# Kernel tuning notes

Measured on AMD Instinct MI355X. Metric: run time of the kernel, lower is better.

## Reference

```python
import jax, jax.numpy as jnp
import numpy as np

B, BAG, H, C = 512, 32, 1024, 53
EPS = 1e-8  # torch F.cosine_similarity denominator clamp


def setup_inputs() -> dict:
    key = jax.random.key(0)
    ks = jax.random.split(key, 5)
    return {
        "sent_reps": jax.random.normal(ks[0], (B, BAG, H), jnp.float32),
        "aug_sent_reps": jax.random.normal(ks[1], (B, BAG, H), jnp.float32),
        "rel_table": jax.random.normal(ks[2], (C, H), jnp.float32),
        "cls_w": jax.random.normal(ks[3], (C, H), jnp.float32) * 0.02,
        "cls_b": jnp.zeros((C,), jnp.float32),
        "labels": jax.random.randint(ks[4], (B,), 0, C),
        "temperature": jnp.asarray(0.1, jnp.float32),
    }


def _cl(rep, aug, bag_rep, T):
    # rep, aug: (B, bag, H); bag_rep: (B, H)
    nr = jnp.linalg.norm(rep, axis=-1)        # (B, bag)
    na = jnp.linalg.norm(aug, axis=-1)        # (B, bag)
    nb = jnp.linalg.norm(bag_rep, axis=-1)    # (B,)
    pos_sim = jnp.sum(rep * aug, axis=-1) / jnp.maximum(nr * na, EPS)  # (B, bag)
    pos = jnp.exp(pos_sim / T)
    # pair[c, j, b] = cos(rep[b, j], bag_rep[c])  -- matches torch permute/broadcast chain
    dots = jnp.einsum('bjh,ch->cjb', rep, bag_rep)               # (B, bag, B)
    denom = jnp.maximum(nb[:, None, None] * nr.T[None], EPS)      # (B, bag, B)
    pair = dots / denom
    idx = jnp.arange(rep.shape[0])
    axis_sim = pair[idx, :, idx]                                  # (B, bag): cos(rep[b,j], bag_rep[b])
    neg = jnp.exp(pair / T).sum(axis=2) - jnp.exp(axis_sim / T)   # (B, bag)
    return jnp.mean(-jnp.log(pos / (pos + neg)))


def reference(sent_reps, aug_sent_reps, rel_table, cls_w, cls_b, labels, temperature):
    # Selective attention per bag (scope slices are uniform bags of size BAG -> vectorized)
    rel = rel_table[labels]                                        # (B, H)
    scale = jnp.sqrt(jnp.asarray(H, sent_reps.dtype))
    scores = jnp.einsum('bh,bjh->bj', rel, sent_reps) / scale      # (B, bag)
    alphas = jax.nn.softmax(scores, axis=-1)
    bag_reps = jnp.einsum('bj,bjh->bh', alphas, sent_reps)         # (B, H)
    bag_out = bag_reps @ cls_w.T + cls_b                           # (B, C)  (dropout in eval = identity)
    cl_loss = _cl(sent_reps, aug_sent_reps, bag_reps, temperature)
    return bag_out, cl_loss
```

## Files before the change

### kernel.cpp

```cpp
#include <hip/hip_runtime.h>
#include <hip/hip_bf16.h>


typedef __bf16 bf16x8 __attribute__((ext_vector_type(8)));
typedef __bf16 bf16x4 __attribute__((ext_vector_type(4)));
typedef __bf16 bf16x2 __attribute__((ext_vector_type(2)));
typedef float  f32x4  __attribute__((ext_vector_type(4)));

__device__ inline float wsum(float v) {
    #pragma unroll
    for (int off = 32; off > 0; off >>= 1) v += __shfl_xor(v, off, 64);
    return v;
}

__device__ inline void gll16(const void* g, void* l) {
    __builtin_amdgcn_global_load_lds((const __attribute__((address_space(1))) void*)g,
                                     (__attribute__((address_space(3))) void*)l, 16, 0, 0);
}

__device__ inline f32x4 ntld(const float* p) {
    return __builtin_nontemporal_load((const f32x4*)p);
}

__global__ __launch_bounds__(512, 4) void kab(
    const float* __restrict__ sent, const float* __restrict__ aug,
    const float* __restrict__ rel_table, const int* __restrict__ labels,
    __bf16* __restrict__ repb, float* __restrict__ nr, float* __restrict__ pos_sim,
    const float* __restrict__ clsw, __bf16* __restrict__ cwb,
    __bf16* __restrict__ bagb, float* __restrict__ nbsq, float* __restrict__ loss)
{
    __shared__ __align__(16) __bf16 repS[32][1024];
    __shared__ float scoreS[32], alphaS[32], redS[8];
    const int b = blockIdx.x, t = threadIdx.x;
    const int w = t >> 6, lane = t & 63;

    if (b < 128) {
        const int i = b * 512 + t;
        cwb[i] = (i < 53 * 1024) ? (__bf16)clsw[i] : (__bf16)0.0f;
        if (b == 0 && t == 0) *loss = 0.0f;
    }

    const float* relp = rel_table + (size_t)labels[b] * 1024;
    #pragma unroll
    for (int rr = 0; rr < 4; rr++) {
        const int j = w * 4 + rr;
        const size_t rbase = ((size_t)b * 32 + j) * 1024;
        const float* srow = sent + rbase;
        const float* arow = aug + rbase;
        float P = 0.f, R = 0.f, A = 0.f, D = 0.f;
        #pragma unroll
        for (int i = 0; i < 4; i++) {
            const int h = i * 256 + lane * 4;
            f32x4 v  = ntld(srow + h);
            f32x4 a  = ntld(arow + h);
            f32x4 rl = *(const f32x4*)(relp + h);
            P += v.x * rl.x + v.y * rl.y + v.z * rl.z + v.w * rl.w;
            R += v.x * v.x + v.y * v.y + v.z * v.z + v.w * v.w;
            A += a.x * a.x + a.y * a.y + a.z * a.z + a.w * a.w;
            D += v.x * a.x + v.y * a.y + v.z * a.z + v.w * a.w;
            bf16x4 vb = { (__bf16)v.x, (__bf16)v.y, (__bf16)v.z, (__bf16)v.w };
            *(bf16x4*)(&repS[j][h]) = vb;
            *(bf16x4*)(repb + rbase + h) = vb;
        }
        #pragma unroll
        for (int off = 32; off > 0; off >>= 1) {
            P += __shfl_xor(P, off, 64);
            R += __shfl_xor(R, off, 64);
            A += __shfl_xor(A, off, 64);
            D += __shfl_xor(D, off, 64);
        }
        if (lane == 0) {
            scoreS[j] = P * (1.0f / 32.0f);
            float nrv = sqrtf(R), nav = sqrtf(A);
            nr[b * 32 + j] = nrv;
            pos_sim[b * 32 + j] = D / fmaxf(nrv * nav, 1e-8f);
        }
    }
    __syncthreads();

    if (t < 32) {
        float sj = scoreS[t], mx = sj;
        #pragma unroll
        for (int off = 16; off > 0; off >>= 1) mx = fmaxf(mx, __shfl_xor(mx, off, 32));
        float e = __expf(sj - mx), sm = e;
        #pragma unroll
        for (int off = 16; off > 0; off >>= 1) sm += __shfl_xor(sm, off, 32);
        alphaS[t] = e / sm;
    }
    __syncthreads();

    float b0 = 0.f, b1 = 0.f;
    #pragma unroll 8
    for (int j = 0; j < 32; j++) {
        const float al = alphaS[j];
        bf16x2 v = *(const bf16x2*)(&repS[j][t * 2]);
        b0 += al * (float)v.x;
        b1 += al * (float)v.y;
    }
    bf16x2 bb = { (__bf16)b0, (__bf16)b1 };
    *(bf16x2*)(bagb + (size_t)b * 1024 + t * 2) = bb;

    float q = b0 * b0 + b1 * b1;
    q = wsum(q);
    if (lane == 0) redS[w] = q;
    __syncthreads();
    if (t == 0)
        nbsq[b] = redS[0] + redS[1] + redS[2] + redS[3]
                + redS[4] + redS[5] + redS[6] + redS[7];
}

__global__ __launch_bounds__(512, 4) void k4_gemm(
    const __bf16* __restrict__ repb, const __bf16* __restrict__ bagb,
    const float* __restrict__ nr, const float* __restrict__ nbsq,
    const float* __restrict__ temp, float* __restrict__ partial, float* __restrict__ diag,
    const __bf16* __restrict__ cwb, const float* __restrict__ bias, float* __restrict__ out)
{
    __shared__ __align__(16) char smem[65536];
    const int bid = blockIdx.x;
    const int t = threadIdx.x, lane = t & 63, w = t >> 6;
    const int m = lane & 15, quad = lane >> 4;

    if (bid >= 512) {
        __bf16* Al = (__bf16*)smem;
        __bf16* Bl = (__bf16*)(smem + 8192);
        const int r0 = (bid - 512) * 64;
        f32x4 acc[4] = {};
        const int i0 = (t & 255) * 8;
        const int row0 = i0 >> 5, kk0 = i0 & 31;
        const __bf16* gA = bagb + (size_t)(r0 + row0) * 1024 + kk0;
        const __bf16* gB = cwb + (size_t)row0 * 1024 + kk0;
        const bool act = (t < 256);
        for (int k0 = 0; k0 < 1024; k0 += 64) {
            __syncthreads();
            if (act) {
                gll16(gA + k0,      Al + i0);
                gll16(gA + k0 + 32, Al + 2048 + i0);
                gll16(gB + k0,      Bl + i0);
                gll16(gB + k0 + 32, Bl + 2048 + i0);
            }
            __syncthreads();
            if (act) {
                #pragma unroll
                for (int ks = 0; ks < 2; ks++) {
                    bf16x8 a = *(const bf16x8*)(&Al[ks * 2048 + (w * 16 + m) * 32 + quad * 8]);
                    #pragma unroll
                    for (int n = 0; n < 4; n++) {
                        bf16x8 bf = *(const bf16x8*)(&Bl[ks * 2048 + (n * 16 + m) * 32 + quad * 8]);
                        acc[n] = __builtin_amdgcn_mfma_f32_16x16x32_bf16(a, bf, acc[n], 0, 0, 0);
                    }
                }
            }
        }
        if (act) {
            #pragma unroll
            for (int n = 0; n < 4; n++) {
                const int c = n * 16 + m;
                if (c < 53) {
                    #pragma unroll
                    for (int i = 0; i < 4; i++) {
                        const int r = r0 + w * 16 + quad * 4 + i;
                        out[(size_t)r * 53 + c] = acc[n][i] + bias[c];
                    }
                }
            }
        }
        return;
    }

    float (*negp)[32][128] = (float (*)[32][128])(smem + 32768);

    const int xcd = bid & 7, slot = bid >> 3;
    const int cb = slot & 3, rb = (slot >> 2) * 8 + xcd;
    const int r0 = rb * 128, c0 = cb * 128;
    const int wr0 = (w & 1) * 64, wc0 = (w >> 1) * 32;
    const int half = w & 1;

    const int tt = t & 255;
    const bool isB = (t >= 256);
    const int srow = tt >> 2;
    const int scol = 8 * ((tt & 3) ^ ((srow >> 1) & 3));
    const __bf16* g0 = (isB ? bagb + (size_t)(c0 + srow) * 1024
                            : repb + (size_t)(r0 + srow) * 1024) + scol;
    const __bf16* g1 = g0 + 64 * 1024;
    const int d0 = (isB ? 4096 : 0) + tt * 8;
    const int d1 = d0 + 2048;

    const int rho = (m >> 1) & 3;
    const int offA = ((wr0 + m) * 4 + (quad ^ rho)) * 8;
    const int offB = 4096 + ((wc0 + m) * 4 + (quad ^ rho)) * 8;

    f32x4 acc[4][2] = {};

    #define BUFB(s) ((__bf16*)(smem + (((s) & 3) << 14)))
    #define STG(s) do { const int kk_ = (s) * 32; __bf16* b_ = BUFB(s);     \
        gll16(g0 + kk_, b_ + d0); gll16(g1 + kk_, b_ + d1); } while (0)

    #define CMP(s) do { const __bf16* b_ = BUFB(s); bf16x8 av_[4], bv_[2];  \
        _Pragma("unroll") for (int i_ = 0; i_ < 4; i_++)                    \
            av_[i_] = *(const bf16x8*)(b_ + offA + i_ * 512);               \
        _Pragma("unroll") for (int n_ = 0; n_ < 2; n_++)                    \
            bv_[n_] = *(const bf16x8*)(b_ + offB + n_ * 512);               \
        _Pragma("unroll") for (int i_ = 0; i_ < 4; i_++)                    \
        _Pragma("unroll") for (int n_ = 0; n_ < 2; n_++)                    \
            acc[i_][n_] = __builtin_amdgcn_mfma_f32_16x16x32_bf16(          \
                av_[i_], bv_[n_], acc[i_][n_], 0, 0, 0); } while (0)

    #define FENCE(N) do { __builtin_amdgcn_sched_barrier(0);                \
        asm volatile("s_waitcnt vmcnt(" #N ")" ::: "memory");               \
        __builtin_amdgcn_s_barrier();                                       \
        __builtin_amdgcn_sched_barrier(0); } while (0)

    STG(0); STG(1); STG(2);
    FENCE(4);
    #pragma unroll 1
    for (int s = 0; s < 29; ++s) {
        STG(s + 3);
        CMP(s);
        FENCE(4);
    }
    CMP(29); FENCE(2);
    CMP(30); FENCE(0);
    CMP(31);
    __syncthreads();

    const float invT = 1.0f / *temp;
    float nrv[16];
    #pragma unroll
    for (int i = 0; i < 4; i++)
        #pragma unroll
        for (int g = 0; g < 4; g++)
            nrv[i * 4 + g] = nr[r0 + wr0 + i * 16 + quad * 4 + g];

    #pragma unroll
    for (int n = 0; n < 2; n++) {
        const int c_local = wc0 + n * 16 + m;
        const int cg = c0 + c_local;
        const float nbv = sqrtf(nbsq[cg]);
        #pragma unroll
        for (int i = 0; i < 2; i++) {
            #pragma unroll
            for (int g = 0; g < 4; g++) {
                const int jj = i * 16 + quad * 4 + g;
                const int rg0 = r0 + wr0 + i * 16 + quad * 4 + g;
                const int rg2 = rg0 + 32;
                float e0 = __expf(acc[i][n][g]     / fmaxf(nbv * nrv[i * 4 + g],       1e-8f) * invT);
                float e2 = __expf(acc[i + 2][n][g] / fmaxf(nbv * nrv[(i + 2) * 4 + g], 1e-8f) * invT);
                negp[half][jj][c_local] = e0 + e2;
                if ((rg0 >> 5) == cg) diag[(size_t)cg * 32 + jj] = e0;
                if ((rg2 >> 5) == cg) diag[(size_t)cg * 32 + jj] = e2;
            }
        }
    }
    __syncthreads();

    float* pout = partial + (size_t)rb * 32 * 512 + c0;
    #pragma unroll
    for (int v = 0; v < 2; v++) {
        const int idx = v * 2048 + t * 4;
        const int jj = idx >> 7, cl = idx & 127;
        f32x4 a = *(const f32x4*)(&negp[0][jj][cl]);
        f32x4 bq = *(const f32x4*)(&negp[1][jj][cl]);
        f32x4 s = a + bq;
        *(f32x4*)(pout + (size_t)jj * 512 + cl) = s;
    }
    #undef BUFB
    #undef STG
    #undef CMP
    #undef FENCE
}

__global__ __launch_bounds__(256) void k5_neg(
    const float* __restrict__ partial, const float* __restrict__ diag,
    const float* __restrict__ pos_sim, const float* __restrict__ temp,
    float* __restrict__ loss)
{
    const int ct = blockIdx.x & 7, j = blockIdx.x >> 3;
    const int t = threadIdx.x, lane = t & 63, w = t >> 6;
    const int bsub = t >> 4;
    const int cidx = t & 15;
    f32x4 acc = {};
    #pragma unroll 4
    for (int r = 0; r < 8; r++) {
        const int rb = bsub * 8 + r;
        f32x4 v = *(const f32x4*)(partial + ((size_t)rb * 32 + j) * 512 + ct * 64 + cidx * 4);
        acc += v;
    }
    #pragma unroll
    for (int k = 0; k < 4; k++) {
        acc[k] += __shfl_xor(acc[k], 16, 64);
        acc[k] += __shfl_xor(acc[k], 32, 64);
    }
    __shared__ float red[4][64];
    if (lane < 16) {
        #pragma unroll
        for (int k = 0; k < 4; k++) red[w][lane * 4 + k] = acc[k];
    }
    __syncthreads();

    if (t < 64) {
        const int c = ct * 64 + t;
        float S = red[0][t] + red[1][t] + red[2][t] + red[3][t];
        S -= diag[(size_t)c * 32 + j];
        const float invT = 1.0f / *temp;
        const float lp = pos_sim[(c << 5) + j] * invT;
        float term = logf(__expf(lp) + S) - lp;
        term = wsum(term);
        if (t == 0) atomicAdd(loss, term * (1.0f / 16384.0f));
    }
}

extern "C" void kernel_launch(void* const* d_in, const int* in_sizes, int n_in,
                              void* d_out, int out_size, void* d_ws, size_t ws_size,
                              hipStream_t stream)
{
    const float* sent = (const float*)d_in[0];
    const float* aug  = (const float*)d_in[1];
    const float* rel  = (const float*)d_in[2];
    const float* clsw = (const float*)d_in[3];
    const float* clsb = (const float*)d_in[4];
    const int*   lab  = (const int*)d_in[5];
    const float* temp = (const float*)d_in[6];
    float* out = (float*)d_out;

    char* ws = (char*)d_ws;
    __bf16* bagb    = (__bf16*)(ws);
    float*  nbsq    = (float*)(ws + (1u << 20));
    float*  nr      = (float*)(ws + (1u << 20) + 64 * 1024);
    float*  pos     = (float*)(ws + (1u << 20) + 128 * 1024);
    __bf16* cwb     = (__bf16*)(ws + (1u << 20) + 192 * 1024);
    float*  diag    = (float*)(ws + (2u << 20) + 64 * 1024);
    __bf16* repb    = (__bf16*)(ws + (4u << 20));
    float*  partial = (float*)(ws + (36u << 20));

    float* loss = out + 27136;

    kab    <<<512, 512, 0, stream>>>(sent, aug, rel, lab, repb, nr, pos,
                                     clsw, cwb, bagb, nbsq, loss);
    k4_gemm<<<520, 512, 0, stream>>>(repb, bagb, nr, nbsq, temp, partial, diag,
                                     cwb, clsb, out);
    k5_neg <<<256, 256, 0, stream>>>(partial, diag, pos, temp, loss);
}
```

Before: 193.6 us.

## Enlarge similarity GEMM tile to 256x128 with 4x4 MFMA per wave

```diff
diff --git a/kernel.cpp b/kernel.cpp
--- a/kernel.cpp
+++ b/kernel.cpp
@@ -109,21 +109,21 @@
                 + redS[4] + redS[5] + redS[6] + redS[7];
 }
 
-__global__ __launch_bounds__(512, 4) void k4_gemm(
+__global__ __launch_bounds__(512, 2) void k4_gemm(
     const __bf16* __restrict__ repb, const __bf16* __restrict__ bagb,
     const float* __restrict__ nr, const float* __restrict__ nbsq,
     const float* __restrict__ temp, float* __restrict__ partial, float* __restrict__ diag,
     const __bf16* __restrict__ cwb, const float* __restrict__ bias, float* __restrict__ out)
 {
-    __shared__ __align__(16) char smem[65536];
+    __shared__ __align__(16) char smem[98304];
     const int bid = blockIdx.x;
     const int t = threadIdx.x, lane = t & 63, w = t >> 6;
     const int m = lane & 15, quad = lane >> 4;
 
-    if (bid >= 512) {
+    if (bid >= 256) {
         __bf16* Al = (__bf16*)smem;
         __bf16* Bl = (__bf16*)(smem + 8192);
-        const int r0 = (bid - 512) * 64;
+        const int r0 = (bid - 256) * 64;
         f32x4 acc[4] = {};
         const int i0 = (t & 255) * 8;
         const int row0 = i0 >> 5, kk0 = i0 & 31;
@@ -142,7 +142,7 @@
             if (act) {
                 #pragma unroll
                 for (int ks = 0; ks < 2; ks++) {
-                    bf16x8 a = *(const bf16x8*)(&Al[ks * 2048 + (w * 16 + m) * 32 + quad * 8]);
+                    bf16x8 a = *(const bf16x8*)(&Al[ks * 2048 + ((t >> 6) * 16 + m) * 32 + quad * 8]);
                     #pragma unroll
                     for (int n = 0; n < 4; n++) {
                         bf16x8 bf = *(const bf16x8*)(&Bl[ks * 2048 + (n * 16 + m) * 32 + quad * 8]);
@@ -158,7 +158,7 @@
                 if (c < 53) {
                     #pragma unroll
                     for (int i = 0; i < 4; i++) {
-                        const int r = r0 + w * 16 + quad * 4 + i;
+                        const int r = r0 + (t >> 6) * 16 + quad * 4 + i;
                         out[(size_t)r * 53 + c] = acc[n][i] + bias[c];
                     }
                 }
@@ -167,41 +167,38 @@
         return;
     }
 
-    float (*negp)[32][128] = (float (*)[32][128])(smem + 32768);
+    float* negp4 = (float*)smem;
 
     const int xcd = bid & 7, slot = bid >> 3;
     const int cb = slot & 3, rb = (slot >> 2) * 8 + xcd;
-    const int r0 = rb * 128, c0 = cb * 128;
-    const int wr0 = (w & 1) * 64, wc0 = (w >> 1) * 32;
-    const int half = w & 1;
-
-    const int tt = t & 255;
-    const bool isB = (t >= 256);
-    const int srow = tt >> 2;
-    const int scol = 8 * ((tt & 3) ^ ((srow >> 1) & 3));
-    const __bf16* g0 = (isB ? bagb + (size_t)(c0 + srow) * 1024
-                            : repb + (size_t)(r0 + srow) * 1024) + scol;
-    const __bf16* g1 = g0 + 64 * 1024;
-    const int d0 = (isB ? 4096 : 0) + tt * 8;
-    const int d1 = d0 + 2048;
+    const int r0 = rb * 256, c0 = cb * 128;
+    const int wr0 = (w & 3) * 64, wc0 = (w >> 2) * 64;
+
+    const int srow = t >> 2;
+    const int scol = 8 * ((t & 3) ^ ((t >> 3) & 3));
+    const __bf16* gA0 = repb + (size_t)(r0 + srow) * 1024 + scol;
+    const __bf16* gA1 = gA0 + (size_t)128 * 1024;
+    const __bf16* gB0 = bagb + (size_t)(c0 + srow) * 1024 + scol;
+    const int dA0 = t * 8, dA1 = (t + 512) * 8, dB0 = 8192 + t * 8;
 
     const int rho = (m >> 1) & 3;
     const int offA = ((wr0 + m) * 4 + (quad ^ rho)) * 8;
-    const int offB = 4096 + ((wc0 + m) * 4 + (quad ^ rho)) * 8;
-
-    f32x4 acc[4][2] = {};
-
-    #define BUFB(s) ((__bf16*)(smem + (((s) & 3) << 14)))
+    const int offB = 8192 + ((wc0 + m) * 4 + (quad ^ rho)) * 8;
+
+    f32x4 acc[4][4] = {};
+
+    #define BUFB(s) ((__bf16*)(smem + (((s) & 3) * 24576)))
     #define STG(s) do { const int kk_ = (s) * 32; __bf16* b_ = BUFB(s);     \
-        gll16(g0 + kk_, b_ + d0); gll16(g1 + kk_, b_ + d1); } while (0)
-
-    #define CMP(s) do { const __bf16* b_ = BUFB(s); bf16x8 av_[4], bv_[2];  \
+        gll16(gA0 + kk_, b_ + dA0); gll16(gA1 + kk_, b_ + dA1);             \
+        gll16(gB0 + kk_, b_ + dB0); } while (0)
+
+    #define CMP(s) do { const __bf16* b_ = BUFB(s); bf16x8 av_[4], bv_[4];  \
         _Pragma("unroll") for (int i_ = 0; i_ < 4; i_++)                    \
             av_[i_] = *(const bf16x8*)(b_ + offA + i_ * 512);               \
-        _Pragma("unroll") for (int n_ = 0; n_ < 2; n_++)                    \
+        _Pragma("unroll") for (int n_ = 0; n_ < 4; n_++)                    \
             bv_[n_] = *(const bf16x8*)(b_ + offB + n_ * 512);               \
         _Pragma("unroll") for (int i_ = 0; i_ < 4; i_++)                    \
-        _Pragma("unroll") for (int n_ = 0; n_ < 2; n_++)                    \
+        _Pragma("unroll") for (int n_ = 0; n_ < 4; n_++)                    \
             acc[i_][n_] = __builtin_amdgcn_mfma_f32_16x16x32_bf16(          \
                 av_[i_], bv_[n_], acc[i_][n_], 0, 0, 0); } while (0)
 
@@ -211,17 +208,16 @@
         __builtin_amdgcn_sched_barrier(0); } while (0)
 
     STG(0); STG(1); STG(2);
-    FENCE(4);
+    FENCE(6);
     #pragma unroll 1
     for (int s = 0; s < 29; ++s) {
         STG(s + 3);
         CMP(s);
-        FENCE(4);
-    }
-    CMP(29); FENCE(2);
+        FENCE(6);
+    }
+    CMP(29); FENCE(3);
     CMP(30); FENCE(0);
     CMP(31);
-    __syncthreads();
 
     const float invT = 1.0f / *temp;
     float nrv[16];
@@ -231,8 +227,9 @@
         for (int g = 0; g < 4; g++)
             nrv[i * 4 + g] = nr[r0 + wr0 + i * 16 + quad * 4 + g];
 
-    #pragma unroll
-    for (int n = 0; n < 2; n++) {
+    float* myneg = negp4 + (size_t)(w & 3) * 32 * 128;
+    #pragma unroll
+    for (int n = 0; n < 4; n++) {
         const int c_local = wc0 + n * 16 + m;
         const int cg = c0 + c_local;
         const float nbv = sqrtf(nbsq[cg]);
@@ -245,7 +242,7 @@
                 const int rg2 = rg0 + 32;
                 float e0 = __expf(acc[i][n][g]     / fmaxf(nbv * nrv[i * 4 + g],       1e-8f) * invT);
                 float e2 = __expf(acc[i + 2][n][g] / fmaxf(nbv * nrv[(i + 2) * 4 + g], 1e-8f) * invT);
-                negp[half][jj][c_local] = e0 + e2;
+                myneg[jj * 128 + c_local] = e0 + e2;
                 if ((rg0 >> 5) == cg) diag[(size_t)cg * 32 + jj] = e0;
                 if ((rg2 >> 5) == cg) diag[(size_t)cg * 32 + jj] = e2;
             }
@@ -254,14 +251,17 @@
     __syncthreads();
 
     float* pout = partial + (size_t)rb * 32 * 512 + c0;
-    #pragma unroll
-    for (int v = 0; v < 2; v++) {
-        const int idx = v * 2048 + t * 4;
-        const int jj = idx >> 7, cl = idx & 127;
-        f32x4 a = *(const f32x4*)(&negp[0][jj][cl]);
-        f32x4 bq = *(const f32x4*)(&negp[1][jj][cl]);
-        f32x4 s = a + bq;
-        *(f32x4*)(pout + (size_t)jj * 512 + cl) = s;
+    {
+        const int jj = t >> 4, c8 = (t & 15) * 8;
+        f32x4 v0 = {}, v1 = {};
+        #pragma unroll
+        for (int p = 0; p < 4; p++) {
+            const float* src = negp4 + (size_t)p * 32 * 128 + jj * 128 + c8;
+            v0 += *(const f32x4*)(src);
+            v1 += *(const f32x4*)(src + 4);
+        }
+        *(f32x4*)(pout + (size_t)jj * 512 + c8)     = v0;
+        *(f32x4*)(pout + (size_t)jj * 512 + c8 + 4) = v1;
     }
     #undef BUFB
     #undef STG
@@ -279,9 +279,9 @@
     const int bsub = t >> 4;
     const int cidx = t & 15;
     f32x4 acc = {};
-    #pragma unroll 4
-    for (int r = 0; r < 8; r++) {
-        const int rb = bsub * 8 + r;
+    #pragma unroll
+    for (int r = 0; r < 4; r++) {
+        const int rb = bsub * 4 + r;
         f32x4 v = *(const f32x4*)(partial + ((size_t)rb * 32 + j) * 512 + ct * 64 + cidx * 4);
         acc += v;
     }
@@ -336,7 +336,7 @@
 
     kab    <<<512, 512, 0, stream>>>(sent, aug, rel, lab, repb, nr, pos,
                                      clsw, cwb, bagb, nbsq, loss);
-    k4_gemm<<<520, 512, 0, stream>>>(repb, bagb, nr, nbsq, temp, partial, diag,
+    k4_gemm<<<264, 512, 0, stream>>>(repb, bagb, nr, nbsq, temp, partial, diag,
                                      cwb, clsb, out);
     k5_neg <<<256, 256, 0, stream>>>(partial, diag, pos, temp, loss);
 }
```

After: 197.6 us. +2.1%, slower.
